# Optimization experiments

Hardware: AMD Instinct MI355X
Metric: run time of the kernel (lower is better)

Reference implementation:

```python
import jax, jax.numpy as jnp
import numpy as np
from jax import lax

BETA = 0.3

def setup_inputs() -> dict:
    key = jax.random.key(0)
    ks = jax.random.split(key, 5)
    B, C, H, W = 1, 64, 96, 96
    x = jax.random.normal(ks[0], (B, C, H, W), dtype=jnp.float32)
    # d_conv: Conv2d(C, C, k=3, stride=1, padding=2, dilation=2)
    dW = jax.random.normal(ks[1], (C, C, 3, 3), dtype=jnp.float32) * 0.05
    db = jax.random.normal(ks[2], (C,), dtype=jnp.float32) * 0.05
    # conv: Conv2d(C, C, k=1)
    cW = jax.random.normal(ks[3], (C, C, 1, 1), dtype=jnp.float32) * 0.1
    cb = jax.random.normal(ks[4], (C,), dtype=jnp.float32) * 0.05
    return {"x": x, "dW": dW, "db": db, "cW": cW, "cb": cb}

def _conv(x, w, b, padding, dilation):
    y = lax.conv_general_dilated(
        x, w, window_strides=(1, 1),
        padding=[(padding, padding), (padding, padding)],
        rhs_dilation=(dilation, dilation),
        dimension_numbers=("NCHW", "OIHW", "NCHW"))
    return y + b[None, :, None, None]

def reference(x, dW, db, cW, cb):
    B, C, H, W = x.shape
    HW = H * W
    y = _conv(x, dW, db, padding=2, dilation=2)   # (B,C,H,W), same d_conv used for q and k
    v = _conv(x, cW, cb, padding=0, dilation=1).reshape(B, HW, C)
    # NOTE: torch uses raw .reshape (not transpose) for q — faithful here.
    q = y.reshape(B, HW, C)
    k = y.reshape(B, C, HW)
    qk = jnp.einsum("bnc,bcm->bnm", q, k)         # (B,HW,HW)
    qk = jnp.where(jnp.abs(qk) > BETA, qk, 0.0)   # threshold mask (qk*mask)
    att = jax.nn.softmax(qk, axis=-1)
    att = jnp.einsum("bnm,bmc->bnc", att, v)      # (B,HW,C)
    att = att.swapaxes(1, 2).reshape(B, C, H, W)
    return x + att
```

## Files before the change

kernel.cpp:

```cpp
#include <hip/hip_runtime.h>
#include <hip/hip_bf16.h>

#define CC 64
#define HW 9216
#define IMG 96
#define SPLITS 8
#define SPLEN 1152
#define ITERS 18
#define LOG2E 1.44269504f

typedef _Float16 f16;
typedef __attribute__((ext_vector_type(8))) _Float16 f16x8;
typedef __attribute__((ext_vector_type(4))) _Float16 f16x4;
typedef __attribute__((ext_vector_type(4))) float f32x4;
typedef __attribute__((ext_vector_type(16))) float f32x16;

__global__ __launch_bounds__(256) void prepad_kernel(
    const float* __restrict__ x, f16* __restrict__ xt)
{
    __shared__ float tile[64][65];
    const int p0 = blockIdx.x * 64;
    const int t = threadIdx.x;
    const int pl = t & 63;
    const int p = p0 + pl;
    int r = p / 100, c = p % 100;
    bool interior = (r >= 2) && (r < 98) && (c >= 2) && (c < 98);
    int img = (r - 2) * IMG + (c - 2);
    #pragma unroll
    for (int j = 0; j < 16; ++j) {
        int ci = j * 4 + (t >> 6);
        tile[pl][ci] = interior ? x[ci * HW + img] : 0.f;
    }
    __syncthreads();
    const int row16 = t >> 4, chunk = t & 15;
    #pragma unroll
    for (int j = 0; j < 4; ++j) {
        int row = j * 16 + row16;
        int pr = p0 + row;
        if (pr < 10000) {
            f16x4 hv = {(f16)tile[row][chunk * 4 + 0], (f16)tile[row][chunk * 4 + 1],
                        (f16)tile[row][chunk * 4 + 2], (f16)tile[row][chunk * 4 + 3]};
            *(f16x4*)&xt[pr * 64 + chunk * 4] = hv;
        }
    }
}

__global__ __launch_bounds__(256) void conv_mfma_kernel(
    const f16* __restrict__ xt, const float* __restrict__ dW, const float* __restrict__ db,
    const float* __restrict__ cW, const float* __restrict__ cb,
    f16* __restrict__ yq, f16* __restrict__ kt, f16* __restrict__ vt)
{
    __shared__ f16 Wl[9 * 16 * 64];
    __shared__ f16 cWl[16 * 64];

    const int b = blockIdx.x;
    const int mblk = b >> 2, cog = b & 3;
    const int co0 = cog * 16;
    const int t = threadIdx.x;

    #pragma unroll 4
    for (int j = 0; j < 36; ++j) {
        int d = j * 256 + t;
        float val = dW[co0 * 576 + d];
        int co  = d / 576;
        int r   = d - co * 576;
        int ci  = r / 9;
        int tap = r - ci * 9;
        Wl[tap * 1024 + co * 64 + ci] = (f16)val;
    }
    #pragma unroll
    for (int j = 0; j < 4; ++j) {
        int d = j * 256 + t;
        cWl[d] = (f16)cW[co0 * CC + d];
    }
    __syncthreads();

    const int w = t >> 6, L = t & 63, g = L >> 4, c16 = L & 15;
    const int ms = mblk * 64 + w * 16;
    const int h = ms / IMG, wc = ms % IMG;
    const int pb = (h + 2) * 100 + (wc + 2) + c16;

    f16x8 Bf[9][2], Bv[2];
    #pragma unroll
    for (int tap = 0; tap < 9; ++tap)
        #pragma unroll
        for (int kc = 0; kc < 2; ++kc)
            Bf[tap][kc] = *(const f16x8*)&Wl[(tap * 16 + c16) * 64 + g * 8 + kc * 32];
    #pragma unroll
    for (int kc = 0; kc < 2; ++kc)
        Bv[kc] = *(const f16x8*)&cWl[c16 * 64 + g * 8 + kc * 32];

    f32x4 accY = (f32x4){0.f, 0.f, 0.f, 0.f};
    f32x4 accV = (f32x4){0.f, 0.f, 0.f, 0.f};

    #pragma unroll
    for (int tap = 0; tap < 9; ++tap) {
        int kh = tap / 3, kw = tap % 3;
        int toff = (2 * kh - 2) * 100 + (2 * kw - 2);
        const f16* ap = xt + (pb + toff) * 64;
        f16x8 A0 = *(const f16x8*)(ap + g * 8);
        f16x8 A1 = *(const f16x8*)(ap + g * 8 + 32);
        accY = __builtin_amdgcn_mfma_f32_16x16x32_f16(A0, Bf[tap][0], accY, 0, 0, 0);
        accY = __builtin_amdgcn_mfma_f32_16x16x32_f16(A1, Bf[tap][1], accY, 0, 0, 0);
        if (tap == 4) {
            accV = __builtin_amdgcn_mfma_f32_16x16x32_f16(A0, Bv[0], accV, 0, 0, 0);
            accV = __builtin_amdgcn_mfma_f32_16x16x32_f16(A1, Bv[1], accV, 0, 0, 0);
        }
    }

    const float dbv = db[co0 + c16], cbv = cb[co0 + c16];
    f16 hy[4];
    #pragma unroll
    for (int j = 0; j < 4; ++j) hy[j] = (f16)(accY[j] + dbv);
    *(f16x4*)&yq[(co0 + c16) * HW + ms + 4 * g] = (f16x4){hy[0], hy[1], hy[2], hy[3]};
    #pragma unroll
    for (int j = 0; j < 4; ++j)
        kt[(ms + 4 * g + j) * 64 + co0 + c16] = hy[j];
    #pragma unroll
    for (int j = 0; j < 4; ++j) {
        int m = ms + 4 * g + j;
        vt[(m & 63) * HW + (co0 + c16) * 144 + (m >> 6)] = (f16)(accV[j] + cbv);
    }
}

__global__ __launch_bounds__(256, 3) void attn_kernel(
    const f16* __restrict__ kt, const f16* __restrict__ vt, const f16* __restrict__ yq,
    f16* __restrict__ acc_ws, float* __restrict__ m_ws, float* __restrict__ l_ws)
{
    __shared__ f16 sKT[64 * 72];
    __shared__ f16 sVT[64 * 72];
    __shared__ f16 sPS[4 * 32 * 72];
    __shared__ float sAL[4 * 32];

    const int t = threadIdx.x;
    const int L = t & 63, w = t >> 6;
    const int l5 = L >> 5, l31 = L & 31;
    const int qb = blockIdx.x >> 3, sp = blockIdx.x & 7;
    const int n0 = qb * 128;
    const int mbase = sp * SPLEN;
    f16* psw = (f16*)sPS + w * 32 * 72;
    float* alw = (float*)sAL + w * 32;

    f16x8 qf[4];
    #pragma unroll
    for (int kc = 0; kc < 4; ++kc)
        qf[kc] = *(const f16x8*)(yq + (n0 + w * 32 + l31) * 64 + kc * 16 + l5 * 8);

    float mi = -1e30f, li = 0.f;
    f32x16 acc[2];
    #pragma unroll
    for (int ct = 0; ct < 2; ++ct)
        #pragma unroll
        for (int r = 0; r < 16; ++r) acc[ct][r] = 0.f;

    for (int it = 0; it < ITERS; ++it) {
        const int m0 = mbase + it * 64;
        __syncthreads();
        #pragma unroll
        for (int rep = 0; rep < 2; ++rep) {
            int idx = t + rep * 256;
            int row = idx >> 3, ch = idx & 7;
            *(uint4*)&sKT[row * 72 + ch * 8] = *(const uint4*)&kt[(m0 + row) * 64 + ch * 8];
            *(uint4*)&sVT[row * 72 + ch * 8] = *(const uint4*)&vt[row * HW + m0 + ch * 8];
        }
        __syncthreads();

        f32x16 st[2];
        #pragma unroll
        for (int kt2 = 0; kt2 < 2; ++kt2) {
            f32x16 d;
            #pragma unroll
            for (int r = 0; r < 16; ++r) d[r] = 0.f;
            #pragma unroll
            for (int kc = 0; kc < 4; ++kc) {
                f16x8 af = *(const f16x8*)&sKT[(kt2 * 32 + l31) * 72 + kc * 16 + l5 * 8];
                d = __builtin_amdgcn_mfma_f32_32x32x16_f16(af, qf[kc], d, 0, 0, 0);
            }
            st[kt2] = d;
        }
        #pragma unroll
        for (int kt2 = 0; kt2 < 2; ++kt2)
            #pragma unroll
            for (int r = 0; r < 16; ++r)
                st[kt2][r] = (fabsf(st[kt2][r]) > 0.3f) ? st[kt2][r] : 0.f;

        float q8[8];
        #pragma unroll
        for (int kt2 = 0; kt2 < 2; ++kt2)
            #pragma unroll
            for (int rq = 0; rq < 4; ++rq)
                q8[kt2 * 4 + rq] = fmaxf(fmaxf(st[kt2][rq * 4 + 0], st[kt2][rq * 4 + 1]),
                                         fmaxf(st[kt2][rq * 4 + 2], st[kt2][rq * 4 + 3]));
        float mx = fmaxf(fmaxf(fmaxf(q8[0], q8[1]), fmaxf(q8[2], q8[3])),
                         fmaxf(fmaxf(q8[4], q8[5]), fmaxf(q8[6], q8[7])));
        mx = fmaxf(mx, __shfl_xor(mx, 32, 64));
        float mnew = fmaxf(mi, mx);
        unsigned long long inc = __ballot(mnew > mi);
        float nL = mnew * LOG2E;

        float ls = 0.f;
        #pragma unroll
        for (int kt2 = 0; kt2 < 2; ++kt2)
            #pragma unroll
            for (int rq = 0; rq < 4; ++rq) {
                float p0 = __builtin_amdgcn_exp2f(fmaf(st[kt2][rq * 4 + 0], LOG2E, -nL));
                float p1 = __builtin_amdgcn_exp2f(fmaf(st[kt2][rq * 4 + 1], LOG2E, -nL));
                float p2 = __builtin_amdgcn_exp2f(fmaf(st[kt2][rq * 4 + 2], LOG2E, -nL));
                float p3 = __builtin_amdgcn_exp2f(fmaf(st[kt2][rq * 4 + 3], LOG2E, -nL));
                ls += (p0 + p1) + (p2 + p3);
                unsigned u0 = __builtin_bit_cast(unsigned int, __builtin_amdgcn_cvt_pkrtz(p0, p1));
                unsigned u1 = __builtin_bit_cast(unsigned int, __builtin_amdgcn_cvt_pkrtz(p2, p3));
                uint2 uv; uv.x = u0; uv.y = u1;
                *(uint2*)&psw[l31 * 72 + kt2 * 32 + rq * 8 + l5 * 4] = uv;
            }

        if (inc) {
            float alpha = __builtin_amdgcn_exp2f(mi * LOG2E - nL);
            li = li * alpha + ls;
            if (l5 == 0) alw[l31] = alpha;
            f32x4 aj[4];
            #pragma unroll
            for (int rq = 0; rq < 4; ++rq)
                aj[rq] = *(const f32x4*)&alw[rq * 8 + l5 * 4];
            #pragma unroll
            for (int ct = 0; ct < 2; ++ct)
                #pragma unroll
                for (int r = 0; r < 16; ++r)
                    acc[ct][r] *= aj[r >> 2][r & 3];
        } else {
            li += ls;
        }
        mi = mnew;

        f16x8 pa[4];
        #pragma unroll
        for (int kc = 0; kc < 4; ++kc)
            pa[kc] = *(const f16x8*)&psw[l31 * 72 + kc * 16 + l5 * 8];
        #pragma unroll
        for (int ct = 0; ct < 2; ++ct)
            #pragma unroll
            for (int kc = 0; kc < 4; ++kc) {
                f16x8 vb = *(const f16x8*)&sVT[(ct * 32 + l31) * 72 + kc * 16 + l5 * 8];
                acc[ct] = __builtin_amdgcn_mfma_f32_32x32x16_f16(pa[kc], vb, acc[ct], 0, 0, 0);
            }
    }

    float li_tot = li + __shfl_xor(li, 32, 64);

    const int base = blockIdx.x;
    #pragma unroll
    for (int ct = 0; ct < 2; ++ct)
        #pragma unroll
        for (int r = 0; r < 16; ++r) {
            int ql = w * 32 + (r & 3) + 8 * (r >> 2) + 4 * l5;
            int c  = ct * 32 + l31;
            acc_ws[base * 8192 + ql * 64 + c] = (f16)acc[ct][r];
        }
    if (l5 == 0) {
        m_ws[base * 128 + w * 32 + l31] = mi;
        l_ws[base * 128 + w * 32 + l31] = li_tot;
    }
}

__global__ __launch_bounds__(256) void merge_kernel(
    const f16* __restrict__ acc_ws, const float* __restrict__ m_ws, const float* __restrict__ l_ws,
    const float* __restrict__ x, float* __restrict__ out)
{
    __shared__ float wsh[SPLITS * 16];
    __shared__ float att[64 * 17];
    const int b = blockIdx.x;
    const int row0 = b * 16;
    const int qb = row0 >> 7;
    const int ql0 = row0 & 127;
    const int t = threadIdx.x;
    if (t < 16) {
        int ql = ql0 + t;
        float ms = -1e30f;
        float mv[SPLITS];
        #pragma unroll
        for (int sp = 0; sp < SPLITS; ++sp) {
            mv[sp] = m_ws[(qb * SPLITS + sp) * 128 + ql];
            ms = fmaxf(ms, mv[sp]);
        }
        float Lsum = 0.f, ev[SPLITS];
        #pragma unroll
        for (int sp = 0; sp < SPLITS; ++sp) {
            ev[sp] = __builtin_amdgcn_exp2f((mv[sp] - ms) * LOG2E);
            Lsum += l_ws[(qb * SPLITS + sp) * 128 + ql] * ev[sp];
        }
        float inv = 1.f / Lsum;
        #pragma unroll
        for (int sp = 0; sp < SPLITS; ++sp)
            wsh[sp * 16 + t] = ev[sp] * inv;
    }
    __syncthreads();
    for (int i = t; i < 1024; i += 256) {
        int rr = i >> 6, c = i & 63;
        float v = 0.f;
        #pragma unroll
        for (int sp = 0; sp < SPLITS; ++sp)
            v += (float)acc_ws[(qb * SPLITS + sp) * 8192 + (ql0 + rr) * 64 + c] * wsh[sp * 16 + rr];
        att[c * 17 + rr] = v;
    }
    __syncthreads();
    for (int i = t; i < 1024; i += 256) {
        int c = i >> 4, r = i & 15;
        int idx = c * HW + row0 + r;
        out[idx] = x[idx] + att[c * 17 + r];
    }
}

extern "C" void kernel_launch(void* const* d_in, const int* in_sizes, int n_in,
                              void* d_out, int out_size, void* d_ws, size_t ws_size,
                              hipStream_t stream)
{
    const float* x  = (const float*)d_in[0];
    const float* dW = (const float*)d_in[1];
    const float* db = (const float*)d_in[2];
    const float* cW = (const float*)d_in[3];
    const float* cb = (const float*)d_in[4];
    float* out = (float*)d_out;

    char* ws = (char*)d_ws;
    f16* kt     = (f16*)(ws);
    f16* yq     = (f16*)(ws + 1179648);
    f16* vt     = (f16*)(ws + 2359296);
    f16* xt     = (f16*)(ws + 3538944);
    f16* acc_ws = (f16*)(ws + 4818944);
    float* m_ws = (float*)(ws + 14256128);
    float* l_ws = (float*)(ws + 14551040);

    prepad_kernel<<<dim3(157), dim3(256), 0, stream>>>(x, xt);
    conv_mfma_kernel<<<dim3(576), dim3(256), 0, stream>>>(xt, dW, db, cW, cb, yq, kt, vt);
    attn_kernel<<<dim3(72 * SPLITS), dim3(256), 0, stream>>>(kt, vt, yq, acc_ws, m_ws, l_ws);
    merge_kernel<<<dim3(576), dim3(256), 0, stream>>>(acc_ws, m_ws, l_ws, x, out);
}
```

Baseline: 137.4 us.

## Register-resident P via permlane swap, swizzled LDS, more splits, pretransposed weights

The attention kernel now builds the P operand in registers with permlane32_swap instead of round-tripping through a per-wave LDS buffer. K and V tiles use an XOR-swizzled unpadded LDS layout to avoid bank conflicts, and launch bounds raise occupancy to 4 blocks. Splits double to 16 with half the KV length each, for more parallelism at the cost of a larger merge workload. The conv weights are converted to f16 once in the prepad kernel, so each conv block no longer transposes them in shared memory.

After: 136.3 us. Within noise of the previous version (-0.7%).

```diff
diff --git a/kernel.cpp b/kernel.cpp
--- a/kernel.cpp
+++ b/kernel.cpp
@@ -4,9 +4,9 @@
 #define CC 64
 #define HW 9216
 #define IMG 96
-#define SPLITS 8
-#define SPLEN 1152
-#define ITERS 18
+#define SPLITS 16
+#define SPLEN 576
+#define ITERS 9
 #define LOG2E 1.44269504f
 
 typedef _Float16 f16;
@@ -14,13 +14,33 @@
 typedef __attribute__((ext_vector_type(4))) _Float16 f16x4;
 typedef __attribute__((ext_vector_type(4))) float f32x4;
 typedef __attribute__((ext_vector_type(16))) float f32x16;
+typedef __attribute__((ext_vector_type(4))) unsigned int u32x4;
 
 __global__ __launch_bounds__(256) void prepad_kernel(
-    const float* __restrict__ x, f16* __restrict__ xt)
+    const float* __restrict__ x, const float* __restrict__ dW, const float* __restrict__ cW,
+    f16* __restrict__ xt, f16* __restrict__ dWt, f16* __restrict__ cWt)
 {
     __shared__ float tile[64][65];
+    const int t = threadIdx.x;
+    if (blockIdx.x >= 157) {
+        const int wb = blockIdx.x - 157;
+        #pragma unroll
+        for (int j = 0; j < 4; ++j) {
+            int idx = wb * 1024 + j * 256 + t;
+            if (idx < 36864) {
+                float val = dW[idx];
+                int co = idx / 576;
+                int r = idx - co * 576;
+                int ci = r / 9, tap = r - ci * 9;
+                dWt[tap * 4096 + co * 64 + ci] = (f16)val;
+            } else {
+                int c = idx - 36864;
+                cWt[c] = (f16)cW[c];
+            }
+        }
+        return;
+    }
     const int p0 = blockIdx.x * 64;
-    const int t = threadIdx.x;
     const int pl = t & 63;
     const int p = p0 + pl;
     int r = p / 100, c = p % 100;
@@ -46,49 +66,29 @@
 }
 
 __global__ __launch_bounds__(256) void conv_mfma_kernel(
-    const f16* __restrict__ xt, const float* __restrict__ dW, const float* __restrict__ db,
-    const float* __restrict__ cW, const float* __restrict__ cb,
+    const f16* __restrict__ xt, const f16* __restrict__ dWt, const float* __restrict__ db,
+    const f16* __restrict__ cWt, const float* __restrict__ cb,
     f16* __restrict__ yq, f16* __restrict__ kt, f16* __restrict__ vt)
 {
-    __shared__ f16 Wl[9 * 16 * 64];
-    __shared__ f16 cWl[16 * 64];
-
     const int b = blockIdx.x;
     const int mblk = b >> 2, cog = b & 3;
     const int co0 = cog * 16;
     const int t = threadIdx.x;
-
-    #pragma unroll 4
-    for (int j = 0; j < 36; ++j) {
-        int d = j * 256 + t;
-        float val = dW[co0 * 576 + d];
-        int co  = d / 576;
-        int r   = d - co * 576;
-        int ci  = r / 9;
-        int tap = r - ci * 9;
-        Wl[tap * 1024 + co * 64 + ci] = (f16)val;
-    }
-    #pragma unroll
-    for (int j = 0; j < 4; ++j) {
-        int d = j * 256 + t;
-        cWl[d] = (f16)cW[co0 * CC + d];
-    }
-    __syncthreads();
-
     const int w = t >> 6, L = t & 63, g = L >> 4, c16 = L & 15;
+
+    f16x8 Bf[9][2], Bv[2];
+    #pragma unroll
+    for (int tap = 0; tap < 9; ++tap)
+        #pragma unroll
+        for (int kc = 0; kc < 2; ++kc)
+            Bf[tap][kc] = *(const f16x8*)&dWt[(tap * 64 + co0 + c16) * 64 + g * 8 + kc * 32];
+    #pragma unroll
+    for (int kc = 0; kc < 2; ++kc)
+        Bv[kc] = *(const f16x8*)&cWt[(co0 + c16) * 64 + g * 8 + kc * 32];
+
     const int ms = mblk * 64 + w * 16;
     const int h = ms / IMG, wc = ms % IMG;
     const int pb = (h + 2) * 100 + (wc + 2) + c16;
-
-    f16x8 Bf[9][2], Bv[2];
-    #pragma unroll
-    for (int tap = 0; tap < 9; ++tap)
-        #pragma unroll
-        for (int kc = 0; kc < 2; ++kc)
-            Bf[tap][kc] = *(const f16x8*)&Wl[(tap * 16 + c16) * 64 + g * 8 + kc * 32];
-    #pragma unroll
-    for (int kc = 0; kc < 2; ++kc)
-        Bv[kc] = *(const f16x8*)&cWl[c16 * 64 + g * 8 + kc * 32];
 
     f32x4 accY = (f32x4){0.f, 0.f, 0.f, 0.f};
     f32x4 accV = (f32x4){0.f, 0.f, 0.f, 0.f};
@@ -123,22 +123,21 @@
     }
 }
 
-__global__ __launch_bounds__(256, 3) void attn_kernel(
+__global__ __launch_bounds__(256, 4) void attn_kernel(
     const f16* __restrict__ kt, const f16* __restrict__ vt, const f16* __restrict__ yq,
     f16* __restrict__ acc_ws, float* __restrict__ m_ws, float* __restrict__ l_ws)
 {
-    __shared__ f16 sKT[64 * 72];
-    __shared__ f16 sVT[64 * 72];
-    __shared__ f16 sPS[4 * 32 * 72];
+    __shared__ f16 sKT[64 * 64];
+    __shared__ f16 sVT[64 * 64];
     __shared__ float sAL[4 * 32];
 
     const int t = threadIdx.x;
     const int L = t & 63, w = t >> 6;
     const int l5 = L >> 5, l31 = L & 31;
-    const int qb = blockIdx.x >> 3, sp = blockIdx.x & 7;
+    const int x7 = l31 & 7;
+    const int qb = blockIdx.x >> 4, sp = blockIdx.x & (SPLITS - 1);
     const int n0 = qb * 128;
     const int mbase = sp * SPLEN;
-    f16* psw = (f16*)sPS + w * 32 * 72;
     float* alw = (float*)sAL + w * 32;
 
     f16x8 qf[4];
@@ -160,8 +159,9 @@
         for (int rep = 0; rep < 2; ++rep) {
             int idx = t + rep * 256;
             int row = idx >> 3, ch = idx & 7;
-            *(uint4*)&sKT[row * 72 + ch * 8] = *(const uint4*)&kt[(m0 + row) * 64 + ch * 8];
-            *(uint4*)&sVT[row * 72 + ch * 8] = *(const uint4*)&vt[row * HW + m0 + ch * 8];
+            int dst = row * 64 + ((ch ^ (row & 7)) << 3);
+            *(uint4*)&sKT[dst] = *(const uint4*)&kt[(m0 + row) * 64 + ch * 8];
+            *(uint4*)&sVT[dst] = *(const uint4*)&vt[row * HW + m0 + ch * 8];
         }
         __syncthreads();
 
@@ -173,7 +173,7 @@
             for (int r = 0; r < 16; ++r) d[r] = 0.f;
             #pragma unroll
             for (int kc = 0; kc < 4; ++kc) {
-                f16x8 af = *(const f16x8*)&sKT[(kt2 * 32 + l31) * 72 + kc * 16 + l5 * 8];
+                f16x8 af = *(const f16x8*)&sKT[(kt2 * 32 + l31) * 64 + ((((kc << 1) | l5) ^ x7) << 3)];
                 d = __builtin_amdgcn_mfma_f32_32x32x16_f16(af, qf[kc], d, 0, 0, 0);
             }
             st[kt2] = d;
@@ -199,6 +199,7 @@
         float nL = mnew * LOG2E;
 
         float ls = 0.f;
+        unsigned int u[2][4][2];
         #pragma unroll
         for (int kt2 = 0; kt2 < 2; ++kt2)
             #pragma unroll
@@ -208,10 +209,8 @@
                 float p2 = __builtin_amdgcn_exp2f(fmaf(st[kt2][rq * 4 + 2], LOG2E, -nL));
                 float p3 = __builtin_amdgcn_exp2f(fmaf(st[kt2][rq * 4 + 3], LOG2E, -nL));
                 ls += (p0 + p1) + (p2 + p3);
-                unsigned u0 = __builtin_bit_cast(unsigned int, __builtin_amdgcn_cvt_pkrtz(p0, p1));
-                unsigned u1 = __builtin_bit_cast(unsigned int, __builtin_amdgcn_cvt_pkrtz(p2, p3));
-                uint2 uv; uv.x = u0; uv.y = u1;
-                *(uint2*)&psw[l31 * 72 + kt2 * 32 + rq * 8 + l5 * 4] = uv;
+                u[kt2][rq][0] = __builtin_bit_cast(unsigned int, __builtin_amdgcn_cvt_pkrtz(p0, p1));
+                u[kt2][rq][1] = __builtin_bit_cast(unsigned int, __builtin_amdgcn_cvt_pkrtz(p2, p3));
             }
 
         if (inc) {
@@ -232,17 +231,24 @@
         }
         mi = mnew;
 
-        f16x8 pa[4];
-        #pragma unroll
-        for (int kc = 0; kc < 4; ++kc)
-            pa[kc] = *(const f16x8*)&psw[l31 * 72 + kc * 16 + l5 * 8];
-        #pragma unroll
-        for (int ct = 0; ct < 2; ++ct)
-            #pragma unroll
-            for (int kc = 0; kc < 4; ++kc) {
-                f16x8 vb = *(const f16x8*)&sVT[(ct * 32 + l31) * 72 + kc * 16 + l5 * 8];
-                acc[ct] = __builtin_amdgcn_mfma_f32_32x32x16_f16(pa[kc], vb, acc[ct], 0, 0, 0);
+        #pragma unroll
+        for (int kc = 0; kc < 4; ++kc) {
+            const int kt2 = kc >> 1;
+            const int rq0 = (kc & 1) * 2, rq1 = rq0 + 1;
+            auto rA = __builtin_amdgcn_permlane32_swap(
+                (int)u[kt2][rq0][0], (int)u[kt2][rq1][0], false, false);
+            auto rB = __builtin_amdgcn_permlane32_swap(
+                (int)u[kt2][rq0][1], (int)u[kt2][rq1][1], false, false);
+            u32x4 pw = {(unsigned int)rA[0], (unsigned int)rB[0],
+                        (unsigned int)rA[1], (unsigned int)rB[1]};
+            f16x8 pa = __builtin_bit_cast(f16x8, pw);
+            #pragma unroll
+            for (int ct = 0; ct < 2; ++ct) {
+                int vrow = ct * 32 + l31;
+                f16x8 vb = *(const f16x8*)&sVT[vrow * 64 + ((((kc << 1) | l5) ^ x7) << 3)];
+                acc[ct] = __builtin_amdgcn_mfma_f32_32x32x16_f16(pa, vb, acc[ct], 0, 0, 0);
             }
+        }
     }
 
     float li_tot = li + __shfl_xor(li, 32, 64);
@@ -326,12 +332,14 @@
     f16* yq     = (f16*)(ws + 1179648);
     f16* vt     = (f16*)(ws + 2359296);
     f16* xt     = (f16*)(ws + 3538944);
-    f16* acc_ws = (f16*)(ws + 4818944);
-    float* m_ws = (float*)(ws + 14256128);
-    float* l_ws = (float*)(ws + 14551040);
-
-    prepad_kernel<<<dim3(157), dim3(256), 0, stream>>>(x, xt);
-    conv_mfma_kernel<<<dim3(576), dim3(256), 0, stream>>>(xt, dW, db, cW, cb, yq, kt, vt);
+    f16* dWt    = (f16*)(ws + 4818944);
+    f16* cWt    = (f16*)(ws + 4892672);
+    f16* acc_ws = (f16*)(ws + 4900864);
+    float* m_ws = (float*)(ws + 23775232);
+    float* l_ws = (float*)(ws + 24365056);
+
+    prepad_kernel<<<dim3(197), dim3(256), 0, stream>>>(x, dW, cW, xt, dWt, cWt);
+    conv_mfma_kernel<<<dim3(576), dim3(256), 0, stream>>>(xt, dWt, db, cWt, cb, yq, kt, vt);
     attn_kernel<<<dim3(72 * SPLITS), dim3(256), 0, stream>>>(kt, vt, yq, acc_ws, m_ws, l_ws);
     merge_kernel<<<dim3(576), dim3(256), 0, stream>>>(acc_ws, m_ws, l_ws, x, out);
 }
```
